# Optimization experiments

Hardware: AMD Instinct MI355X
Metric: run time of the kernel (lower is better)

Reference implementation:

```python
import jax, jax.numpy as jnp
import numpy as np

# Module constants derived from default grid_config
D = 59          # depth bins: (60-1)/1
C_OUT = 64
X, Y, Z = 128, 128, 7
STRIDE = 16
GRID_LB = np.array([-51.2, -51.2, -2.5], dtype=np.float32)
GRID_IV = np.array([0.8, 0.8, 1.0], dtype=np.float32)
D0, DSTEP = 1.0, 1.0

B, N, C_IN, H, W = 4, 6, 256, 16, 44


def _voxel_coords():
    xs, ys, zs = np.meshgrid(np.arange(X), np.arange(Y), np.arange(Z), indexing='ij')
    coords = np.stack([xs, ys, zs], axis=-1).reshape(-1, 3).astype(np.float32)
    coords = coords * GRID_IV + GRID_LB  # [V, 3] ego-frame voxel centers
    return coords


def _camera_rig(rng):
    """Realistic 6-camera rig: yawed cameras looking outward, z_cam = forward."""
    c2e = np.zeros((B, N, 4, 4), dtype=np.float32)
    K = np.zeros((B, N, 3, 3), dtype=np.float32)
    for b in range(B):
        for n in range(N):
            a = 2.0 * np.pi * n / N + 0.02 * rng.standard_normal()
            f = np.array([np.cos(a), np.sin(a), 0.0])           # camera forward (z_cam)
            x_cam = np.array([-np.sin(a), np.cos(a), 0.0])      # camera right
            y_cam = np.array([0.0, 0.0, -1.0])                   # camera down
            R = np.stack([x_cam, y_cam, f], axis=1)              # columns = cam axes in ego
            t = 1.0 * f + np.array([0.0, 0.0, 1.5])
            c2e[b, n, :3, :3] = R
            c2e[b, n, :3, 3] = t
            c2e[b, n, 3, 3] = 1.0
            fl = 400.0 + 5.0 * rng.standard_normal()
            K[b, n] = np.array([[fl, 0.0, 352.0], [0.0, fl, 128.0], [0.0, 0.0, 1.0]])
    return c2e, K


def setup_inputs() -> dict:
    key = jax.random.key(0)
    k1, k2, k3 = jax.random.split(key, 3)
    img_feats = jax.random.normal(k1, (B, N, C_IN, H, W), dtype=jnp.float32)
    c2e, K = _camera_rig(np.random.default_rng(0))
    # depth_net: 1x1 conv in_channels -> D + C_OUT
    w_depth = jax.random.normal(k2, (D + C_OUT, C_IN), dtype=jnp.float32) * (1.0 / np.sqrt(C_IN))
    b_depth = jax.random.normal(k3, (D + C_OUT,), dtype=jnp.float32) * 0.01
    return {
        'img_feats': img_feats,
        'cam2ego': jnp.asarray(c2e),
        'cam_intrinsics': jnp.asarray(K),
        'w_depth': w_depth,
        'b_depth': b_depth,
    }


def reference(img_feats, cam2ego, cam_intrinsics, w_depth, b_depth):
    Bc, Nc, C, Hc, Wc = img_feats.shape
    # 1x1 conv == per-pixel linear
    x = jnp.einsum('bnchw,oc->bnhwo', img_feats, w_depth) + b_depth  # [B,N,H,W,D+C_OUT]
    depth = jax.nn.softmax(x[..., :D], axis=-1)                      # [B,N,H,W,D]
    feat = x[..., D:]                                                # [B,N,H,W,C_OUT]

    vox = jnp.asarray(_voxel_coords())                               # [V,3]
    V = vox.shape[0]
    vox_h = jnp.concatenate([vox, jnp.ones((V, 1), vox.dtype)], axis=1)  # [V,4]

    e2c = jnp.linalg.inv(cam2ego)                                    # [B,N,4,4]
    cam = jnp.einsum('bnij,vj->bnvi', e2c, vox_h)[..., :3]           # [B,N,V,3]
    z = cam[..., 2]
    z_safe = jnp.maximum(z, 0.1)
    norm = cam[..., :2] / z_safe[..., None]
    homo = jnp.concatenate([norm, jnp.ones_like(z[..., None])], axis=-1)  # [B,N,V,3]
    img = jnp.einsum('bnij,bnvj->bnvi', cam_intrinsics, homo)[..., :2]
    fc = img / STRIDE                                                # feature-plane coords

    depth_bin = ((z - D0) / DSTEP).astype(jnp.int32)                 # trunc toward 0, matches .long()
    valid = (
        (fc[..., 0] >= 0) & (fc[..., 0] < Wc)
        & (fc[..., 1] >= 0) & (fc[..., 1] < Hc)
        & (z > 0.5)
        & (depth_bin >= 0) & (depth_bin < D)
    )

    u = jnp.clip(fc[..., 0].astype(jnp.int32), 0, Wc - 1)            # [B,N,V]
    v = jnp.clip(fc[..., 1].astype(jnp.int32), 0, Hc - 1)
    d = jnp.clip(depth_bin, 0, D - 1)
    hw = v * Wc + u

    feat_flat = feat.reshape(Bc, Nc, Hc * Wc, C_OUT)
    sampled_feat = jnp.take_along_axis(feat_flat, hw[..., None], axis=2)   # [B,N,V,C_OUT]
    depth_flat = depth.reshape(Bc, Nc, Hc * Wc * D)
    sampled_depth = jnp.take_along_axis(depth_flat, hw * D + d, axis=2)    # [B,N,V]

    wgt = sampled_depth * valid.astype(sampled_depth.dtype)
    # scatter_add at flat_idx == voxel index (identity) -> masked sum over cameras
    bev = jnp.einsum('bnv,bnvc->bvc', wgt, sampled_feat)             # [B,V,C_OUT]
    bev = bev.reshape(Bc, X, Y, Z, C_OUT).sum(axis=3)                # collapse Z
    bev = bev.transpose(0, 3, 2, 1)                                  # [B,C_OUT,Y,X]
    return bev, depth
```

## Files before the change

### kernel.cpp

```cpp
#include <hip/hip_runtime.h>
#include <math.h>

#define D_BINS 59
#define CO     64
#define CI     256
#define NB     4
#define NC     6
#define H_IMG  16
#define W_IMG  44
#define HW     704
#define NPIX   (NB*NC*HW)
#define XD     128
#define YD     128
#define ZD     7
#define NOUT   123
#define PXB    66

typedef float v2f __attribute__((ext_vector_type(2)));

__device__ void inv_rigid(const float* __restrict__ M, float* __restrict__ o) {
    double a = M[0], b = M[1], c = M[2], t0 = M[3];
    double d = M[4], e = M[5], f = M[6], t1 = M[7];
    double g = M[8], h = M[9], ii = M[10], t2 = M[11];
    double A00 = e*ii - f*h, A01 = c*h - b*ii, A02 = b*f - c*e;
    double A10 = f*g - d*ii, A11 = a*ii - c*g, A12 = c*d - a*f;
    double A20 = d*h - e*g,  A21 = b*g - a*h,  A22 = a*e - b*d;
    double det = a*A00 + b*A10 + c*A20;
    double inv = 1.0 / det;
    double r00 = A00*inv, r01 = A01*inv, r02 = A02*inv;
    double r10 = A10*inv, r11 = A11*inv, r12 = A12*inv;
    double r20 = A20*inv, r21 = A21*inv, r22 = A22*inv;
    o[0] = (float)r00; o[1] = (float)r01; o[2]  = (float)r02;
    o[3] = (float)(-(r00*t0 + r01*t1 + r02*t2));
    o[4] = (float)r10; o[5] = (float)r11; o[6]  = (float)r12;
    o[7] = (float)(-(r10*t0 + r11*t1 + r12*t2));
    o[8] = (float)r20; o[9] = (float)r21; o[10] = (float)r22;
    o[11] = (float)(-(r20*t0 + r21*t1 + r22*t2));
}

__global__ __launch_bounds__(256) void k_pre(
    const float* __restrict__ wd, const float* __restrict__ c2e,
    float* __restrict__ wt2, float* __restrict__ e2c) {
    const int o = blockIdx.x;
    const int k = threadIdx.x;
    float v = (o < NOUT) ? wd[(size_t)o * CI + k] : 0.f;
    wt2[(size_t)(k >> 1) * 256 + o * 2 + (k & 1)] = v;
    if (blockIdx.x == 0 && k < NB * NC)
        inv_rigid(c2e + k * 16, e2c + k * 12);
}

__global__ __launch_bounds__(640) void k_head(
    const float* __restrict__ img, const float* __restrict__ wt2,
    const float* __restrict__ bd, float* __restrict__ depth_out,
    float* __restrict__ feat_ws) {
    __shared__ float smem[PXB * 132 + PXB];
    float* S = smem + PXB * 132;

    const int tid = threadIdx.x;
    const int wv  = tid >> 6;
    const int ln  = tid & 63;
    const int p0  = blockIdx.x * PXB;
    const bool is_main = (wv < 8);
    const int o0  = __builtin_amdgcn_readfirstlane((is_main ? wv : 0) << 4);
    const int epx = 64 + (wv - 8);

    v2f acc[16];
#pragma unroll
    for (int j = 0; j < 16; ++j) acc[j] = (v2f)(0.f);
    v2f acc2a = (v2f)(0.f), acc2b = (v2f)(0.f);

    for (int kc = 0; kc < 4; ++kc) {
#pragma unroll
        for (int it = 0; it < 7; ++it) {
            int idx = tid + it * 640;
            if (idx < 64 * PXB) {
                int kl = idx / PXB, px = idx - kl * PXB;
                int p = p0 + px;
                int bn = p / HW, hw = p - bn * HW;
                smem[(kl >> 1) * 132 + px * 2 + (kl & 1)] =
                    img[((size_t)bn * CI + kc * 64 + kl) * HW + hw];
            }
        }
        __syncthreads();
        if (is_main) {
#pragma unroll 4
            for (int k2 = 0; k2 < 32; ++k2) {
                v2f a = *(const v2f*)(smem + k2 * 132 + ln * 2);
                const v2f* w =
                    (const v2f*)(wt2 + (size_t)(kc * 32 + k2) * 256) + o0;
#pragma unroll
                for (int j = 0; j < 16; ++j)
                    acc[j] = __builtin_elementwise_fma(a, w[j], acc[j]);
            }
        } else {
#pragma unroll 4
            for (int k2 = 0; k2 < 32; ++k2) {
                v2f a = *(const v2f*)(smem + k2 * 132 + epx * 2);
                const float* w = wt2 + (size_t)(kc * 32 + k2) * 256;
                v2f w0 = {w[ln * 2], w[ln * 2 + 1]};
                v2f w1 = {w[(ln + 64) * 2], w[(ln + 64) * 2 + 1]};
                acc2a = __builtin_elementwise_fma(a, w0, acc2a);
                acc2b = __builtin_elementwise_fma(a, w1, acc2b);
            }
        }
        __syncthreads();
    }

    float* X = smem;
    if (is_main) {
#pragma unroll
        for (int j = 0; j < 16; ++j) {
            int o = o0 + j;
            if (o < NOUT) {
                int col = (o < D_BINS) ? o : o + 5;
                X[ln * 132 + col] = (acc[j].x + acc[j].y) + bd[o];
            }
        }
    } else {
        int o = ln;
        X[epx * 132 + ((o < D_BINS) ? o : o + 5)] = (acc2a.x + acc2a.y) + bd[o];
        o = ln + 64;
        if (o < NOUT)
            X[epx * 132 + ((o < D_BINS) ? o : o + 5)] = (acc2b.x + acc2b.y) + bd[o];
    }
    __syncthreads();

#pragma unroll
    for (int it = 0; it < 2; ++it) {
        int g = tid + it * 640;
        if (g < PXB * 16) {
            int p = g >> 4, m = g & 15;
            float4 v = *(const float4*)(X + p * 132 + 64 + m * 4);
            *(float4*)(feat_ws + (size_t)(p0 + p) * CO + m * 4) = v;
        }
    }

    if (tid < PXB) {
        float* row = X + tid * 132;
        float m = row[0];
        for (int o = 1; o < D_BINS; ++o) m = fmaxf(m, row[o]);
        float s = 0.f;
        for (int o = 0; o < D_BINS; ++o) {
            float e = __expf(row[o] - m);
            row[o] = e;
            s += e;
        }
        S[tid] = 1.f / s;
    }
    __syncthreads();

    for (int g = tid; g < PXB * D_BINS; g += 640) {
        int p = g / D_BINS;
        int o = g - p * D_BINS;
        depth_out[(size_t)p0 * D_BINS + g] = X[p * 132 + o] * S[p];
    }
}

__global__ __launch_bounds__(256) void k_splat(
    const float* __restrict__ e2c, const float* __restrict__ Kmat,
    const float* __restrict__ depth_g, const float* __restrict__ feat_ws,
    float* __restrict__ bev) {
    __shared__ int   hw_s[ZD][64];
    __shared__ float wgt_s[ZD][64];

    const int tx = threadIdx.x;
    const int cq = threadIdx.y;
    const int x = blockIdx.x * 64 + tx;
    const int y = blockIdx.y;
    const int b = blockIdx.z;
    const float wx = (float)x * 0.8f + (-51.2f);
    const float wy = (float)y * 0.8f + (-51.2f);

    float acc[16];
#pragma unroll
    for (int m = 0; m < 16; ++m) acc[m] = 0.f;

    for (int n = 0; n < NC; ++n) {
        const int bn = b * NC + n;
        const float* E = e2c + bn * 12;
        const float* Km = Kmat + bn * 9;
        const float k00 = Km[0], k01 = Km[1], k02 = Km[2];
        const float k10 = Km[3], k11 = Km[4], k12 = Km[5];
        const float e02 = E[2], e12 = E[6], e22 = E[10];
        const float bx0 = E[0] * wx + E[1] * wy + E[3];
        const float bx1 = E[4] * wx + E[5] * wy + E[7];
        const float bx2 = E[8] * wx + E[9] * wy + E[11];

#pragma unroll
        for (int zz = 0; zz < 2; ++zz) {
            const int z = cq + zz * 4;
            if (z < ZD) {
                const float wz = -2.5f + (float)z;
                const float cx = bx0 + e02 * wz;
                const float cy = bx1 + e12 * wz;
                const float cz = bx2 + e22 * wz;
                const float zs = fmaxf(cz, 0.1f);
                const float rz = 1.0f / zs;
                const float xn = cx * rz;
                const float yn = cy * rz;
                const float fu = (k00 * xn + k01 * yn + k02) * 0.0625f;
                const float fv = (k10 * xn + k11 * yn + k12) * 0.0625f;
                const int bin = (int)(cz - 1.0f);
                const bool valid = (fu >= 0.f) & (fu < (float)W_IMG) &
                                   (fv >= 0.f) & (fv < (float)H_IMG) &
                                   (cz > 0.5f) & (bin >= 0) & (bin < D_BINS);
                int hw = -1;
                float wgt = 0.f;
                if (valid) {
                    int u = (int)fu;
                    int v = (int)fv;
                    hw = v * W_IMG + u;
                    wgt = depth_g[((size_t)bn * HW + hw) * D_BINS + bin];
                }
                hw_s[z][tx] = hw;
                wgt_s[z][tx] = wgt;
            }
        }
        __syncthreads();

#pragma unroll
        for (int z = 0; z < ZD; ++z) {
            const int hw = hw_s[z][tx];
            if (hw >= 0) {
                const float wgt = wgt_s[z][tx];
                const float4* fp =
                    (const float4*)(feat_ws + ((size_t)bn * HW + hw) * CO + cq * 16);
                float4 f0 = fp[0], f1 = fp[1], f2 = fp[2], f3 = fp[3];
                acc[0]  = fmaf(wgt, f0.x, acc[0]);
                acc[1]  = fmaf(wgt, f0.y, acc[1]);
                acc[2]  = fmaf(wgt, f0.z, acc[2]);
                acc[3]  = fmaf(wgt, f0.w, acc[3]);
                acc[4]  = fmaf(wgt, f1.x, acc[4]);
                acc[5]  = fmaf(wgt, f1.y, acc[5]);
                acc[6]  = fmaf(wgt, f1.z, acc[6]);
                acc[7]  = fmaf(wgt, f1.w, acc[7]);
                acc[8]  = fmaf(wgt, f2.x, acc[8]);
                acc[9]  = fmaf(wgt, f2.y, acc[9]);
                acc[10] = fmaf(wgt, f2.z, acc[10]);
                acc[11] = fmaf(wgt, f2.w, acc[11]);
                acc[12] = fmaf(wgt, f3.x, acc[12]);
                acc[13] = fmaf(wgt, f3.y, acc[13]);
                acc[14] = fmaf(wgt, f3.z, acc[14]);
                acc[15] = fmaf(wgt, f3.w, acc[15]);
            }
        }
        __syncthreads();
    }
    float* ob = bev + (((size_t)b * CO + cq * 16) * YD + y) * XD + x;
#pragma unroll
    for (int m = 0; m < 16; ++m) ob[(size_t)m * YD * XD] = acc[m];
}

extern "C" void kernel_launch(void* const* d_in, const int* in_sizes, int n_in,
                              void* d_out, int out_size, void* d_ws, size_t ws_size,
                              hipStream_t stream) {
    const float* img  = (const float*)d_in[0];
    const float* c2e  = (const float*)d_in[1];
    const float* Kmat = (const float*)d_in[2];
    const float* wd   = (const float*)d_in[3];
    const float* bd   = (const float*)d_in[4];
    float* bev = (float*)d_out;
    float* depth_out = bev + (size_t)NB * CO * YD * XD;
    float* feat_ws = (float*)d_ws;
    float* wt2 = feat_ws + (size_t)NPIX * CO;
    float* e2c = wt2 + 128 * 256;

    k_pre<<<128, 256, 0, stream>>>(wd, c2e, wt2, e2c);
    k_head<<<256, 640, 0, stream>>>(img, wt2, bd, depth_out, feat_ws);
    k_splat<<<dim3(2, YD, NB), dim3(64, 4, 1), 0, stream>>>(e2c, Kmat, depth_out,
                                                            feat_ws, bev);
}
```

Baseline: 124.0 us.

## Remap splat threads to channels with wave-uniform voxel gathers and LDS-transposed output

Restructures the splat kernel so each lane owns one output channel and each wave walks 16 x-positions, so feature gathers read 64 contiguous floats per voxel instead of scattered float4 rows. The projected index and weight are packed into one int2 in shared memory and broadcast with readfirstlane, which makes the validity branch wave-uniform. Results are transposed through a padded shared-memory tile so the BEV stores stay coalesced. This adds a shared-memory staging pass and more serial per-lane work per wave in exchange for better gather coalescing.

Result: slower. 212.3 us (+71.1%).

```diff
diff --git a/kernel.cpp b/kernel.cpp
--- a/kernel.cpp
+++ b/kernel.cpp
@@ -160,15 +160,20 @@
     const float* __restrict__ e2c, const float* __restrict__ Kmat,
     const float* __restrict__ depth_g, const float* __restrict__ feat_ws,
     float* __restrict__ bev) {
-    __shared__ int   hw_s[ZD][64];
-    __shared__ float wgt_s[ZD][64];
+    __shared__ int2  proj_s[ZD][64];
+    __shared__ float out_s[64][65];
 
     const int tx = threadIdx.x;
-    const int cq = threadIdx.y;
-    const int x = blockIdx.x * 64 + tx;
-    const int y = blockIdx.y;
-    const int b = blockIdx.z;
-    const float wx = (float)x * 0.8f + (-51.2f);
+    const int ty = threadIdx.y;
+    const int tid = ty * 64 + tx;
+    const int x0 = blockIdx.x * 64;
+    const int y  = blockIdx.y;
+    const int b  = blockIdx.z;
+
+    const int c  = tx;
+    const int wvx = ty * 16;
+
+    const float wx = (float)(x0 + tx) * 0.8f + (-51.2f);
     const float wy = (float)y * 0.8f + (-51.2f);
 
     float acc[16];
@@ -177,78 +182,87 @@
 
     for (int n = 0; n < NC; ++n) {
         const int bn = b * NC + n;
-        const float* E = e2c + bn * 12;
-        const float* Km = Kmat + bn * 9;
-        const float k00 = Km[0], k01 = Km[1], k02 = Km[2];
-        const float k10 = Km[3], k11 = Km[4], k12 = Km[5];
-        const float e02 = E[2], e12 = E[6], e22 = E[10];
-        const float bx0 = E[0] * wx + E[1] * wy + E[3];
-        const float bx1 = E[4] * wx + E[5] * wy + E[7];
-        const float bx2 = E[8] * wx + E[9] * wy + E[11];
-
-#pragma unroll
-        for (int zz = 0; zz < 2; ++zz) {
-            const int z = cq + zz * 4;
-            if (z < ZD) {
-                const float wz = -2.5f + (float)z;
-                const float cx = bx0 + e02 * wz;
-                const float cy = bx1 + e12 * wz;
-                const float cz = bx2 + e22 * wz;
-                const float zs = fmaxf(cz, 0.1f);
-                const float rz = 1.0f / zs;
-                const float xn = cx * rz;
-                const float yn = cy * rz;
-                const float fu = (k00 * xn + k01 * yn + k02) * 0.0625f;
-                const float fv = (k10 * xn + k11 * yn + k12) * 0.0625f;
-                const int bin = (int)(cz - 1.0f);
-                const bool valid = (fu >= 0.f) & (fu < (float)W_IMG) &
-                                   (fv >= 0.f) & (fv < (float)H_IMG) &
-                                   (cz > 0.5f) & (bin >= 0) & (bin < D_BINS);
-                int hw = -1;
-                float wgt = 0.f;
-                if (valid) {
-                    int u = (int)fu;
-                    int v = (int)fv;
-                    hw = v * W_IMG + u;
-                    wgt = depth_g[((size_t)bn * HW + hw) * D_BINS + bin];
+        const size_t bnHW = (size_t)bn * HW;
+
+        {
+            const float* E = e2c + bn * 12;
+            const float* Km = Kmat + bn * 9;
+            const float k00 = Km[0], k01 = Km[1], k02 = Km[2];
+            const float k10 = Km[3], k11 = Km[4], k12 = Km[5];
+            const float e02 = E[2], e12 = E[6], e22 = E[10];
+            const float bx0 = E[0] * wx + E[1] * wy + E[3];
+            const float bx1 = E[4] * wx + E[5] * wy + E[7];
+            const float bx2 = E[8] * wx + E[9] * wy + E[11];
+#pragma unroll
+            for (int zz = 0; zz < 2; ++zz) {
+                const int z = ty + zz * 4;
+                if (z < ZD) {
+                    const float wz = -2.5f + (float)z;
+                    const float cx = bx0 + e02 * wz;
+                    const float cy = bx1 + e12 * wz;
+                    const float cz = bx2 + e22 * wz;
+                    const float zs = fmaxf(cz, 0.1f);
+                    const float rz = 1.0f / zs;
+                    const float xn = cx * rz;
+                    const float yn = cy * rz;
+                    const float fu = (k00 * xn + k01 * yn + k02) * 0.0625f;
+                    const float fv = (k10 * xn + k11 * yn + k12) * 0.0625f;
+                    const int bin = (int)(cz - 1.0f);
+                    const bool valid = (fu >= 0.f) & (fu < (float)W_IMG) &
+                                       (fv >= 0.f) & (fv < (float)H_IMG) &
+                                       (cz > 0.5f) & (bin >= 0) & (bin < D_BINS);
+                    int hw = -1;
+                    float wgt = 0.f;
+                    if (valid) {
+                        int u = (int)fu;
+                        int v = (int)fv;
+                        hw = v * W_IMG + u;
+                        wgt = depth_g[(bnHW + hw) * D_BINS + bin];
+                    }
+                    proj_s[z][tx] = make_int2(hw, __float_as_int(wgt));
                 }
-                hw_s[z][tx] = hw;
-                wgt_s[z][tx] = wgt;
-            }
-        }
-        __syncthreads();
-
-#pragma unroll
-        for (int z = 0; z < ZD; ++z) {
-            const int hw = hw_s[z][tx];
-            if (hw >= 0) {
-                const float wgt = wgt_s[z][tx];
-                const float4* fp =
-                    (const float4*)(feat_ws + ((size_t)bn * HW + hw) * CO + cq * 16);
-                float4 f0 = fp[0], f1 = fp[1], f2 = fp[2], f3 = fp[3];
-                acc[0]  = fmaf(wgt, f0.x, acc[0]);
-                acc[1]  = fmaf(wgt, f0.y, acc[1]);
-                acc[2]  = fmaf(wgt, f0.z, acc[2]);
-                acc[3]  = fmaf(wgt, f0.w, acc[3]);
-                acc[4]  = fmaf(wgt, f1.x, acc[4]);
-                acc[5]  = fmaf(wgt, f1.y, acc[5]);
-                acc[6]  = fmaf(wgt, f1.z, acc[6]);
-                acc[7]  = fmaf(wgt, f1.w, acc[7]);
-                acc[8]  = fmaf(wgt, f2.x, acc[8]);
-                acc[9]  = fmaf(wgt, f2.y, acc[9]);
-                acc[10] = fmaf(wgt, f2.z, acc[10]);
-                acc[11] = fmaf(wgt, f2.w, acc[11]);
-                acc[12] = fmaf(wgt, f3.x, acc[12]);
-                acc[13] = fmaf(wgt, f3.y, acc[13]);
-                acc[14] = fmaf(wgt, f3.z, acc[14]);
-                acc[15] = fmaf(wgt, f3.w, acc[15]);
-            }
-        }
-        __syncthreads();
-    }
-    float* ob = bev + (((size_t)b * CO + cq * 16) * YD + y) * XD + x;
-#pragma unroll
-    for (int m = 0; m < 16; ++m) ob[(size_t)m * YD * XD] = acc[m];
+            }
+        }
+        __syncthreads();
+
+#pragma unroll
+        for (int xp = 0; xp < 8; ++xp) {
+            const int xl0 = wvx + xp * 2;
+            const int xl1 = xl0 + 1;
+            float fv0[ZD], fw0[ZD], fv1[ZD], fw1[ZD];
+#pragma unroll
+            for (int z = 0; z < ZD; ++z) {
+                int2 p0 = proj_s[z][xl0];
+                int hw0 = __builtin_amdgcn_readfirstlane(p0.x);
+                if (hw0 >= 0) {
+                    fw0[z] = __int_as_float(__builtin_amdgcn_readfirstlane(p0.y));
+                    fv0[z] = feat_ws[(bnHW + (size_t)hw0) * CO + c];
+                } else { fw0[z] = 0.f; fv0[z] = 0.f; }
+                int2 p1 = proj_s[z][xl1];
+                int hw1 = __builtin_amdgcn_readfirstlane(p1.x);
+                if (hw1 >= 0) {
+                    fw1[z] = __int_as_float(__builtin_amdgcn_readfirstlane(p1.y));
+                    fv1[z] = feat_ws[(bnHW + (size_t)hw1) * CO + c];
+                } else { fw1[z] = 0.f; fv1[z] = 0.f; }
+            }
+#pragma unroll
+            for (int z = 0; z < ZD; ++z) {
+                acc[xp * 2]     = fmaf(fw0[z], fv0[z], acc[xp * 2]);
+                acc[xp * 2 + 1] = fmaf(fw1[z], fv1[z], acc[xp * 2 + 1]);
+            }
+        }
+        __syncthreads();
+    }
+
+#pragma unroll
+    for (int xi = 0; xi < 16; ++xi)
+        out_s[c][wvx + xi] = acc[xi];
+    __syncthreads();
+
+    for (int g = tid; g < 64 * 64; g += 256) {
+        int cc = g >> 6, xx = g & 63;
+        bev[(((size_t)b * CO + cc) * YD + y) * XD + x0 + xx] = out_s[cc][xx];
+    }
 }
 
 extern "C" void kernel_launch(void* const* d_in, const int* in_sizes, int n_in,
```

## Double-buffer image tile in LDS with register prefetch of next K chunk

Applied to the files above, without the earlier changes.

The 1x1-conv head kernel now precomputes the per-thread shared-memory and global offsets once. It splits LDS into two image-tile buffers and, while computing on one K chunk, loads the next chunk from global memory into registers, then writes it to the other buffer. This hides global load latency behind the FMA loop and drops one barrier per iteration. The cost is extra registers for the prefetched values and offsets, which could lower occupancy.

Result: no change. 124.2 us (+0.1%).

```diff
diff --git a/kernel.cpp b/kernel.cpp
--- a/kernel.cpp
+++ b/kernel.cpp
@@ -15,6 +15,7 @@
 #define ZD     7
 #define NOUT   123
 #define PXB    66
+#define ABUF   4224
 
 typedef float v2f __attribute__((ext_vector_type(2)));
 
@@ -64,28 +65,49 @@
     const int o0  = __builtin_amdgcn_readfirstlane((is_main ? wv : 0) << 4);
     const int epx = 64 + (wv - 8);
 
+    int a_off[7];
+    int g_off[7];
+#pragma unroll
+    for (int it = 0; it < 7; ++it) {
+        int idx = tid + it * 640;
+        if (idx < 64 * PXB) {
+            int kl = idx / PXB, px = idx - kl * PXB;
+            int p = p0 + px;
+            int bn = p / HW, hw = p - bn * HW;
+            a_off[it] = (kl >> 1) * 132 + px * 2 + (kl & 1);
+            g_off[it] = (bn * CI + kl) * HW + hw;
+        } else {
+            a_off[it] = -1;
+            g_off[it] = 0;
+        }
+    }
+
     v2f acc[16];
 #pragma unroll
     for (int j = 0; j < 16; ++j) acc[j] = (v2f)(0.f);
     v2f acc2a = (v2f)(0.f), acc2b = (v2f)(0.f);
 
+#pragma unroll
+    for (int it = 0; it < 7; ++it)
+        if (a_off[it] >= 0) smem[a_off[it]] = img[g_off[it]];
+    __syncthreads();
+
     for (int kc = 0; kc < 4; ++kc) {
-#pragma unroll
-        for (int it = 0; it < 7; ++it) {
-            int idx = tid + it * 640;
-            if (idx < 64 * PXB) {
-                int kl = idx / PXB, px = idx - kl * PXB;
-                int p = p0 + px;
-                int bn = p / HW, hw = p - bn * HW;
-                smem[(kl >> 1) * 132 + px * 2 + (kl & 1)] =
-                    img[((size_t)bn * CI + kc * 64 + kl) * HW + hw];
-            }
-        }
-        __syncthreads();
+        const float* A = smem + (kc & 1) * ABUF;
+        float* An = smem + ((kc + 1) & 1) * ABUF;
+
+        float r[7];
+        if (kc < 3) {
+#pragma unroll
+            for (int it = 0; it < 7; ++it)
+                if (a_off[it] >= 0)
+                    r[it] = img[g_off[it] + (kc + 1) * 64 * HW];
+        }
+
         if (is_main) {
 #pragma unroll 4
             for (int k2 = 0; k2 < 32; ++k2) {
-                v2f a = *(const v2f*)(smem + k2 * 132 + ln * 2);
+                v2f a = *(const v2f*)(A + k2 * 132 + ln * 2);
                 const v2f* w =
                     (const v2f*)(wt2 + (size_t)(kc * 32 + k2) * 256) + o0;
 #pragma unroll
@@ -95,13 +117,19 @@
         } else {
 #pragma unroll 4
             for (int k2 = 0; k2 < 32; ++k2) {
-                v2f a = *(const v2f*)(smem + k2 * 132 + epx * 2);
+                v2f a = *(const v2f*)(A + k2 * 132 + epx * 2);
                 const float* w = wt2 + (size_t)(kc * 32 + k2) * 256;
                 v2f w0 = {w[ln * 2], w[ln * 2 + 1]};
                 v2f w1 = {w[(ln + 64) * 2], w[(ln + 64) * 2 + 1]};
                 acc2a = __builtin_elementwise_fma(a, w0, acc2a);
                 acc2b = __builtin_elementwise_fma(a, w1, acc2b);
             }
+        }
+
+        if (kc < 3) {
+#pragma unroll
+            for (int it = 0; it < 7; ++it)
+                if (a_off[it] >= 0) An[a_off[it]] = r[it];
         }
         __syncthreads();
     }
```

## Split depth-head GEMM output channels across two blocks per pixel tile

Applied to the files above, without the earlier changes.

The head kernel now launches a 2D grid where each block computes 64 of the 123 output channels for a 66-pixel tile, using 384 threads instead of 640. The first half handles the depth logits plus five feature channels and does the softmax; the second half writes the remaining feature channels. The global load offsets for the image tile are precomputed once in registers rather than recomputed for each k-chunk. This doubles the block count for better CU occupancy on the 256-CU-class device, at the cost of loading every image tile twice.

New measurement: 122.5 us (median of 2 runs). About the same (-1.2%).

```diff
diff --git a/kernel.cpp b/kernel.cpp
--- a/kernel.cpp
+++ b/kernel.cpp
@@ -15,6 +15,8 @@
 #define ZD     7
 #define NOUT   123
 #define PXB    66
+#define THR    384
+#define XW     66
 
 typedef float v2f __attribute__((ext_vector_type(2)));
 
@@ -49,43 +51,51 @@
         inv_rigid(c2e + k * 16, e2c + k * 12);
 }
 
-__global__ __launch_bounds__(640) void k_head(
+__global__ __launch_bounds__(THR) void k_head(
     const float* __restrict__ img, const float* __restrict__ wt2,
     const float* __restrict__ bd, float* __restrict__ depth_out,
     float* __restrict__ feat_ws) {
-    __shared__ float smem[PXB * 132 + PXB];
-    float* S = smem + PXB * 132;
-
-    const int tid = threadIdx.x;
-    const int wv  = tid >> 6;
-    const int ln  = tid & 63;
-    const int p0  = blockIdx.x * PXB;
-    const bool is_main = (wv < 8);
-    const int o0  = __builtin_amdgcn_readfirstlane((is_main ? wv : 0) << 4);
-    const int epx = 64 + (wv - 8);
+    __shared__ float A[64 / 2 * 132];
+    __shared__ float X[PXB * XW];
+    __shared__ float S[PXB];
+
+    const int tid  = threadIdx.x;
+    const int wv   = tid >> 6;
+    const int ln   = tid & 63;
+    const int p0   = blockIdx.x * PXB;
+    const int half = blockIdx.y;
+    const int ob   = half << 6;
+    const bool is_main = (wv < 4);
+    const int o0   = __builtin_amdgcn_readfirstlane(ob + ((is_main ? wv : 0) << 4));
+    const int epx  = 64 + (wv - 4);
+
+    int a_off[11];
+    int g_off[11];
+#pragma unroll
+    for (int it = 0; it < 11; ++it) {
+        int idx = tid + it * THR;
+        int kl = idx / PXB, px = idx - kl * PXB;
+        int p = p0 + px;
+        int bn = p / HW, hw = p - bn * HW;
+        a_off[it] = (kl >> 1) * 132 + px * 2 + (kl & 1);
+        g_off[it] = (bn * CI + kl) * HW + hw;
+    }
 
     v2f acc[16];
 #pragma unroll
     for (int j = 0; j < 16; ++j) acc[j] = (v2f)(0.f);
-    v2f acc2a = (v2f)(0.f), acc2b = (v2f)(0.f);
+    v2f acc2 = (v2f)(0.f);
 
     for (int kc = 0; kc < 4; ++kc) {
 #pragma unroll
-        for (int it = 0; it < 7; ++it) {
-            int idx = tid + it * 640;
-            if (idx < 64 * PXB) {
-                int kl = idx / PXB, px = idx - kl * PXB;
-                int p = p0 + px;
-                int bn = p / HW, hw = p - bn * HW;
-                smem[(kl >> 1) * 132 + px * 2 + (kl & 1)] =
-                    img[((size_t)bn * CI + kc * 64 + kl) * HW + hw];
-            }
-        }
-        __syncthreads();
+        for (int it = 0; it < 11; ++it)
+            A[a_off[it]] = img[g_off[it] + kc * 64 * HW];
+        __syncthreads();
+
         if (is_main) {
 #pragma unroll 4
             for (int k2 = 0; k2 < 32; ++k2) {
-                v2f a = *(const v2f*)(smem + k2 * 132 + ln * 2);
+                v2f a = *(const v2f*)(A + k2 * 132 + ln * 2);
                 const v2f* w =
                     (const v2f*)(wt2 + (size_t)(kc * 32 + k2) * 256) + o0;
 #pragma unroll
@@ -95,64 +105,58 @@
         } else {
 #pragma unroll 4
             for (int k2 = 0; k2 < 32; ++k2) {
-                v2f a = *(const v2f*)(smem + k2 * 132 + epx * 2);
+                v2f a = *(const v2f*)(A + k2 * 132 + epx * 2);
                 const float* w = wt2 + (size_t)(kc * 32 + k2) * 256;
-                v2f w0 = {w[ln * 2], w[ln * 2 + 1]};
-                v2f w1 = {w[(ln + 64) * 2], w[(ln + 64) * 2 + 1]};
-                acc2a = __builtin_elementwise_fma(a, w0, acc2a);
-                acc2b = __builtin_elementwise_fma(a, w1, acc2b);
-            }
-        }
-        __syncthreads();
-    }
-
-    float* X = smem;
+                v2f w0 = {w[(ob + ln) * 2], w[(ob + ln) * 2 + 1]};
+                acc2 = __builtin_elementwise_fma(a, w0, acc2);
+            }
+        }
+        __syncthreads();
+    }
+
     if (is_main) {
 #pragma unroll
         for (int j = 0; j < 16; ++j) {
             int o = o0 + j;
-            if (o < NOUT) {
-                int col = (o < D_BINS) ? o : o + 5;
-                X[ln * 132 + col] = (acc[j].x + acc[j].y) + bd[o];
-            }
+            if (o < NOUT)
+                X[ln * XW + (o - ob)] = (acc[j].x + acc[j].y) + bd[o];
         }
     } else {
-        int o = ln;
-        X[epx * 132 + ((o < D_BINS) ? o : o + 5)] = (acc2a.x + acc2a.y) + bd[o];
-        o = ln + 64;
+        int o = ob + ln;
         if (o < NOUT)
-            X[epx * 132 + ((o < D_BINS) ? o : o + 5)] = (acc2b.x + acc2b.y) + bd[o];
+            X[epx * XW + ln] = (acc2.x + acc2.y) + bd[o];
     }
     __syncthreads();
 
-#pragma unroll
-    for (int it = 0; it < 2; ++it) {
-        int g = tid + it * 640;
-        if (g < PXB * 16) {
-            int p = g >> 4, m = g & 15;
-            float4 v = *(const float4*)(X + p * 132 + 64 + m * 4);
-            *(float4*)(feat_ws + (size_t)(p0 + p) * CO + m * 4) = v;
-        }
-    }
-
-    if (tid < PXB) {
-        float* row = X + tid * 132;
-        float m = row[0];
-        for (int o = 1; o < D_BINS; ++o) m = fmaxf(m, row[o]);
-        float s = 0.f;
-        for (int o = 0; o < D_BINS; ++o) {
-            float e = __expf(row[o] - m);
-            row[o] = e;
-            s += e;
-        }
-        S[tid] = 1.f / s;
-    }
-    __syncthreads();
-
-    for (int g = tid; g < PXB * D_BINS; g += 640) {
-        int p = g / D_BINS;
-        int o = g - p * D_BINS;
-        depth_out[(size_t)p0 * D_BINS + g] = X[p * 132 + o] * S[p];
+    if (half == 0) {
+        if (tid < PXB * 5) {
+            int p = tid / 5, c = tid - p * 5;
+            feat_ws[(size_t)(p0 + p) * CO + c] = X[p * XW + 59 + c];
+        }
+        if (tid < PXB) {
+            float* row = X + tid * XW;
+            float m = row[0];
+            for (int o = 1; o < D_BINS; ++o) m = fmaxf(m, row[o]);
+            float s = 0.f;
+            for (int o = 0; o < D_BINS; ++o) {
+                float e = __expf(row[o] - m);
+                row[o] = e;
+                s += e;
+            }
+            S[tid] = 1.f / s;
+        }
+        __syncthreads();
+        for (int g = tid; g < PXB * D_BINS; g += THR) {
+            int p = g / D_BINS;
+            int o = g - p * D_BINS;
+            depth_out[(size_t)p0 * D_BINS + g] = X[p * XW + o] * S[p];
+        }
+    } else {
+        for (int g = tid; g < PXB * D_BINS; g += THR) {
+            int p = g / D_BINS;
+            int col = g - p * D_BINS;
+            feat_ws[(size_t)(p0 + p) * CO + 5 + col] = X[p * XW + col];
+        }
     }
 }
 
@@ -266,7 +270,7 @@
     float* e2c = wt2 + 128 * 256;
 
     k_pre<<<128, 256, 0, stream>>>(wd, c2e, wt2, e2c);
-    k_head<<<256, 640, 0, stream>>>(img, wt2, bd, depth_out, feat_ws);
+    k_head<<<dim3(256, 2), THR, 0, stream>>>(img, wt2, bd, depth_out, feat_ws);
     k_splat<<<dim3(2, YD, NB), dim3(64, 4, 1), 0, stream>>>(e2c, Kmat, depth_out,
                                                             feat_ws, bev);
 }
```
